# Kernel optimization log

Measured on AMD Instinct MI355X. Metric: run time of the kernel, lower is better.

Reference implementation:

```python
import jax, jax.numpy as jnp
import numpy as np

EPS = 1e-4
HEADS = 8
DIM_HEAD = 32
BALANCE = 0.3


def _normalize(x, dims):
    # torch normalize(): norm over `dims` in fp32; norm = eps + norm*sqrt(norm.numel()/x.numel())
    red = 1
    for d in dims:
        red *= x.shape[d]
    norm = jnp.sqrt(jnp.sum(jnp.square(x.astype(jnp.float32)), axis=dims, keepdims=True))
    norm = EPS + norm / np.sqrt(red)
    return x / norm.astype(x.dtype)


def _mpconv1x1(x, w, gain=1.0):
    # MPConv forward (eval mode): weight-normalize per output channel, scale, 1x1 conv
    w = w.astype(jnp.float32)
    w = _normalize(w, (1, 2, 3))
    fan_in = w.shape[1] * w.shape[2] * w.shape[3]
    w = (w * (gain / np.sqrt(fan_in))).astype(x.dtype)[:, :, 0, 0]  # [out, in]
    return jnp.einsum('oi,nihw->nohw', w, x)


def setup_inputs() -> dict:
    key = jax.random.key(0)
    k1, k2, k3 = jax.random.split(key, 3)
    x = jax.random.normal(k1, (2, 256, 48, 48), dtype=jnp.float32)
    w_qkv = jax.random.normal(k2, (768, 256, 1, 1), dtype=jnp.float32)
    w_out = jax.random.normal(k3, (256, 256, 1, 1), dtype=jnp.float32)
    return {"x": x, "w_qkv": w_qkv, "w_out": w_out}


def reference(x, w_qkv, w_out):
    n, c, h, w_sp = x.shape
    seq = h * w_sp
    y = _mpconv1x1(x, w_qkv)                          # [n, 3c, h, w]
    y = y.reshape(n, HEADS, DIM_HEAD, 3, seq)         # channel split: head x dim_head x 3
    y = _normalize(y, (2,))                           # L2-normalize over dim_head axis
    q = y[:, :, :, 0, :]
    k = y[:, :, :, 1, :]
    v = y[:, :, :, 2, :]
    # scores [n, h, q, k] with k scaled by 1/sqrt(dim_head)
    att = jax.nn.softmax(jnp.einsum('nhcq,nhck->nhqk', q, k) / np.sqrt(DIM_HEAD), axis=3)
    y = jnp.einsum('nhqk,nhck->nhcq', att, v)         # [n, heads, dim_head, seq]
    y = _mpconv1x1(y.reshape(n, c, h, w_sp), w_out)
    t = BALANCE
    # mp_sum: lerp then magnitude-preserving rescale
    return (x + t * (y - x)) / np.sqrt((1 - t) ** 2 + t ** 2)
```

## Files before the change

### kernel.cpp

```cpp
#include <hip/hip_runtime.h>
#include <math.h>

#define EPSN 1e-4f
#define SEQ 2304

using bf16x8 = __attribute__((ext_vector_type(8))) short;
using f32x4  = __attribute__((ext_vector_type(4))) float;

__device__ inline unsigned short f2bf(float x) {
    union { float f; unsigned u; } c; c.f = x;
    unsigned u = c.u;
    u += 0x7fffu + ((u >> 16) & 1u);
    return (unsigned short)(u >> 16);
}

__device__ inline unsigned cvt_pk_bf16(float lo, float hi) {
    unsigned r;
    asm("v_cvt_pk_bf16_f32 %0, %1, %2" : "=v"(r) : "v"(lo), "v"(hi));
    return r;
}
__device__ inline void permlane32_swap(unsigned &a, unsigned &b) {
    asm("v_permlane32_swap_b32 %0, %1" : "+v"(a), "+v"(b));
}
__device__ inline void permlane16_swap(unsigned &a, unsigned &b) {
    asm("v_permlane16_swap_b32 %0, %1" : "+v"(a), "+v"(b));
}

__global__ __launch_bounds__(256) void prep_kernel(const float* __restrict__ w_qkv,
                                                   const float* __restrict__ w_out,
                                                   const float* __restrict__ x,
                                                   unsigned short* __restrict__ wqb,
                                                   unsigned short* __restrict__ wob,
                                                   unsigned short* __restrict__ xt) {
    __shared__ __align__(16) unsigned short T[64][80];
    int bid = blockIdx.x;
    if (bid < 256) {
        int wave = threadIdx.x >> 6, lane = threadIdx.x & 63;
        int row = bid * 4 + wave;
        const float* src;
        unsigned short* dst;
        if (row < 768) { src = w_qkv + (size_t)row * 256; dst = wqb + (size_t)row * 256; }
        else           { src = w_out + (size_t)(row - 768) * 256; dst = wob + (size_t)(row - 768) * 256; }
        float4 v = *(const float4*)&src[lane * 4];
        float ss = v.x * v.x + v.y * v.y + v.z * v.z + v.w * v.w;
        for (int off = 32; off > 0; off >>= 1) ss += __shfl_xor(ss, off, 64);
        float sc = 1.0f / (sqrtf(ss) + 16.0f * EPSN);
        unsigned p0 = (unsigned)f2bf(v.x * sc) | ((unsigned)f2bf(v.y * sc) << 16);
        unsigned p1 = (unsigned)f2bf(v.z * sc) | ((unsigned)f2bf(v.w * sc) << 16);
        *(uint2*)&dst[lane * 4] = make_uint2(p0, p1);
    } else {
        int e0 = bid - 256;
        int st = e0 % 36, ct = (e0 / 36) & 3, n = e0 / 144;
        int t = threadIdx.x;
#pragma unroll
        for (int p = 0; p < 4; ++p) {
            int e = t + p * 256;
            int c = e >> 4, sv = (e & 15) * 4;
            float4 v = *(const float4*)&x[(size_t)(n * 256 + ct * 64 + c) * SEQ + st * 64 + sv];
            T[sv + 0][c] = f2bf(v.x);
            T[sv + 1][c] = f2bf(v.y);
            T[sv + 2][c] = f2bf(v.z);
            T[sv + 3][c] = f2bf(v.w);
        }
        __syncthreads();
#pragma unroll
        for (int p = 0; p < 2; ++p) {
            int e = t + p * 256;
            int s = e >> 3, cb = (e & 7) * 8;
            uint4 v = *(const uint4*)&T[s][cb];
            *(uint4*)&xt[(size_t)(n * SEQ + st * 64 + s) * 256 + ct * 64 + cb] = v;
        }
    }
}

__global__ __launch_bounds__(256) void qkv_fused_kernel(const unsigned short* __restrict__ xt,
                                                        const unsigned short* __restrict__ wqb,
                                                        unsigned short* __restrict__ qn,
                                                        unsigned short* __restrict__ kn,
                                                        unsigned short* __restrict__ vn) {
    __shared__ float Cs[96][65];
    __shared__ __align__(16) unsigned short Vls[32][72];
    int h  = blockIdx.x;
    int st = blockIdx.y;
    int n  = blockIdx.z;
    int tid = threadIdx.x;
    int wave = tid >> 6, lane = tid & 63;
    int ln = lane & 15, quad = lane >> 4;
    const unsigned short* Abase = wqb + (size_t)(h * 96 + ln) * 256 + quad * 8;
    const unsigned short* Bbase = xt + (size_t)(n * SEQ + st * 64 + wave * 16 + ln) * 256 + quad * 8;
    f32x4 acc[6];
#pragma unroll
    for (int m = 0; m < 6; ++m) acc[m] = (f32x4){0.f, 0.f, 0.f, 0.f};
#pragma unroll
    for (int kc = 0; kc < 8; ++kc) {
        bf16x8 b = *(const bf16x8*)(Bbase + kc * 32);
#pragma unroll
        for (int m = 0; m < 6; ++m) {
            bf16x8 a = *(const bf16x8*)(Abase + (size_t)(m * 16) * 256 + kc * 32);
            acc[m] = __builtin_amdgcn_mfma_f32_16x16x32_bf16(a, b, acc[m], 0, 0, 0);
        }
    }
#pragma unroll
    for (int m = 0; m < 6; ++m)
#pragma unroll
        for (int r = 0; r < 4; ++r)
            Cs[m * 16 + quad * 4 + r][wave * 16 + ln] = acc[m][r];
    __syncthreads();
    int nh = n * 8 + h;
    if (tid < 192) {
        int sl = tid & 63, wh = tid >> 6;
        int s = st * 64 + sl;
        float v[32];
        float ss = 0.f;
#pragma unroll
        for (int d = 0; d < 32; ++d) { v[d] = Cs[3 * d + wh][sl]; ss += v[d] * v[d]; }
        float inv = 1.0f / (EPSN + sqrtf(ss * (1.0f / 32.0f)));
        if (wh == 0) inv *= 0.17677669529663687f * 1.4426950408889634f;
        if (wh == 2) {
#pragma unroll
            for (int d = 0; d < 32; ++d) Vls[d][sl] = f2bf(v[d] * inv);
        } else {
            unsigned short* dst = (wh == 1 ? kn : qn) + (size_t)nh * 73728 + (size_t)s * 32;
            unsigned wbuf[16];
#pragma unroll
            for (int j = 0; j < 16; ++j)
                wbuf[j] = (unsigned)f2bf(v[2 * j] * inv) | ((unsigned)f2bf(v[2 * j + 1] * inv) << 16);
#pragma unroll
            for (int j = 0; j < 4; ++j) {
                uint4 t4 = make_uint4(wbuf[4 * j], wbuf[4 * j + 1], wbuf[4 * j + 2], wbuf[4 * j + 3]);
                *(uint4*)(dst + j * 8) = t4;
            }
        }
    }
    __syncthreads();
    {
        int d = tid >> 3, sj = (tid & 7) * 8;
        uint4 t4 = *(const uint4*)&Vls[d][sj];
        *(uint4*)&vn[(size_t)nh * 73728 + (size_t)d * SEQ + st * 64 + sj] = t4;
    }
}

__global__ __launch_bounds__(512) void attn_mfma_kernel(const unsigned short* __restrict__ qn,
                                                        const unsigned short* __restrict__ kn,
                                                        const unsigned short* __restrict__ vn,
                                                        unsigned short* __restrict__ y2t) {
    __shared__ __align__(16) unsigned char SM[38912];
    unsigned short (*Ks)[64][40] = (unsigned short (*)[64][40])SM;
    unsigned short (*Vs)[32][72] = (unsigned short (*)[32][72])(SM + 20480);
    int tid = threadIdx.x;
    int wave = tid >> 6, lane = tid & 63;
    int ln = lane & 15, quad = lane >> 4;
    int kg = wave >> 2, wq = wave & 3;
    int bid = blockIdx.x;
    int xcd = bid & 7, bi = bid >> 3;
    int nh = xcd * 2 + (bi >= 36);
    int qt = (bi >= 36) ? bi - 36 : bi;
    int n = nh >> 3, h = nh & 7;
    const unsigned short* Qg = qn + (size_t)nh * 73728;
    const unsigned short* Kg = kn + (size_t)nh * 73728;
    const unsigned short* Vg = vn + (size_t)nh * 73728;

    bf16x8 qf = *(const bf16x8*)(Qg + (size_t)(qt * 64 + wq * 16 + ln) * 32 + quad * 8);
    bf16x8 ones;
#pragma unroll
    for (int i = 0; i < 8; ++i) ones[i] = (short)0x3F80;

    f32x4 o0 = {0.f, 0.f, 0.f, 0.f};
    f32x4 o1 = {0.f, 0.f, 0.f, 0.f};
    f32x4 lac = {0.f, 0.f, 0.f, 0.f};

    int ts = tid & 255;
    int kg2 = kg * 2;
    int s0 = kg * 18 * 64;
    uint4 kreg = *(const uint4*)(Kg + (size_t)s0 * 32 + ts * 8);
    uint4 vreg = *(const uint4*)(Vg + (size_t)(ts >> 3) * SEQ + s0 + (ts & 7) * 8);
    *(uint4*)(&Ks[kg2][ts >> 2][(ts & 3) * 8]) = kreg;
    *(uint4*)(&Vs[kg2][ts >> 3][(ts & 7) * 8]) = vreg;

    for (int i = 0; i < 18; ++i) {
        int buf = i & 1;
        if (i + 1 < 18) {
            int sn = s0 + (i + 1) * 64;
            kreg = *(const uint4*)(Kg + (size_t)sn * 32 + ts * 8);
            vreg = *(const uint4*)(Vg + (size_t)(ts >> 3) * SEQ + sn + (ts & 7) * 8);
        }
        __syncthreads();

        const f32x4 zero = {0.f, 0.f, 0.f, 0.f};
        unsigned w[4][2];
#pragma unroll
        for (int c = 0; c < 4; ++c) {
            bf16x8 kf = *(const bf16x8*)(&Ks[kg2 + buf][c * 16 + ln][quad * 8]);
            f32x4 sc = __builtin_amdgcn_mfma_f32_16x16x32_bf16(kf, qf, zero, 0, 0, 0);
            w[c][0] = cvt_pk_bf16(exp2f(sc[0]), exp2f(sc[1]));
            w[c][1] = cvt_pk_bf16(exp2f(sc[2]), exp2f(sc[3]));
        }
#pragma unroll
        for (int kc = 0; kc < 2; ++kc) {
            unsigned a0 = w[2 * kc][0], b0 = w[2 * kc + 1][0];
            permlane32_swap(a0, b0);
            permlane16_swap(a0, b0);
            unsigned a1 = w[2 * kc][1], b1 = w[2 * kc + 1][1];
            permlane32_swap(a1, b1);
            permlane16_swap(a1, b1);
            union { unsigned u[4]; bf16x8 v8; } pk;
            pk.u[0] = a0; pk.u[1] = a1; pk.u[2] = b0; pk.u[3] = b1;
            bf16x8 v0 = *(const bf16x8*)(&Vs[kg2 + buf][ln][kc * 32 + quad * 8]);
            bf16x8 v1 = *(const bf16x8*)(&Vs[kg2 + buf][16 + ln][kc * 32 + quad * 8]);
            lac = __builtin_amdgcn_mfma_f32_16x16x32_bf16(pk.v8, ones, lac, 0, 0, 0);
            o0  = __builtin_amdgcn_mfma_f32_16x16x32_bf16(pk.v8, v0, o0, 0, 0, 0);
            o1  = __builtin_amdgcn_mfma_f32_16x16x32_bf16(pk.v8, v1, o1, 0, 0, 0);
        }
        if (i + 1 < 18) {
            *(uint4*)(&Ks[kg2 + (buf ^ 1)][ts >> 2][(ts & 3) * 8]) = kreg;
            *(uint4*)(&Vs[kg2 + (buf ^ 1)][ts >> 3][(ts & 7) * 8]) = vreg;
        }
    }

    __syncthreads();
    float (*Os)[36] = (float (*)[36])SM;
    float* Ls = (float*)(SM + 128 * 36 * 4);
#pragma unroll
    for (int r = 0; r < 4; ++r) {
        int q = wq * 16 + quad * 4 + r;
        Os[kg * 64 + q][ln] = o0[r];
        Os[kg * 64 + q][16 + ln] = o1[r];
        if (ln == 0) Ls[kg * 64 + q] = lac[r];
    }
    __syncthreads();
    {
        int q = tid >> 3, dg = (tid & 7) * 4;
        float inv = 1.0f / (Ls[q] + Ls[64 + q]);
        float r0 = (Os[q][dg + 0] + Os[64 + q][dg + 0]) * inv;
        float r1 = (Os[q][dg + 1] + Os[64 + q][dg + 1]) * inv;
        float r2 = (Os[q][dg + 2] + Os[64 + q][dg + 2]) * inv;
        float r3 = (Os[q][dg + 3] + Os[64 + q][dg + 3]) * inv;
        *(uint2*)&y2t[((size_t)(n * SEQ) + qt * 64 + q) * 256 + h * 32 + dg] =
            make_uint2(cvt_pk_bf16(r0, r1), cvt_pk_bf16(r2, r3));
    }
}

__global__ __launch_bounds__(256) void out_gemm_kernel(const unsigned short* __restrict__ y2t,
                                                       const unsigned short* __restrict__ wob,
                                                       const float* __restrict__ x,
                                                       float* __restrict__ out) {
    int mt = blockIdx.x;
    int st = blockIdx.y;
    int n  = blockIdx.z;
    int tid = threadIdx.x;
    int wave = tid >> 6, lane = tid & 63;
    int ln = lane & 15, quad = lane >> 4;
    int m0 = mt * 64 + wave * 16;
    const unsigned short* Abase = wob + (size_t)(m0 + ln) * 256 + quad * 8;
    const unsigned short* Bbase = y2t + (size_t)(n * SEQ + st * 32 + ln) * 256 + quad * 8;
    f32x4 acc[2];
#pragma unroll
    for (int c = 0; c < 2; ++c) acc[c] = (f32x4){0.f, 0.f, 0.f, 0.f};
#pragma unroll
    for (int kc = 0; kc < 8; ++kc) {
        bf16x8 a = *(const bf16x8*)(Abase + kc * 32);
#pragma unroll
        for (int c = 0; c < 2; ++c) {
            bf16x8 b = *(const bf16x8*)(Bbase + (size_t)(c * 16) * 256 + kc * 32);
            acc[c] = __builtin_amdgcn_mfma_f32_16x16x32_bf16(a, b, acc[c], 0, 0, 0);
        }
    }
    const float c0f = 0.7f * 1.3130643285972254f;
    const float c1f = 0.3f * 1.3130643285972254f;
#pragma unroll
    for (int c = 0; c < 2; ++c)
#pragma unroll
        for (int r = 0; r < 4; ++r) {
            int o = m0 + quad * 4 + r;
            int s = st * 32 + c * 16 + ln;
            size_t idx = (size_t)(n * 256 + o) * SEQ + s;
            out[idx] = c0f * x[idx] + c1f * acc[c][r];
        }
}

extern "C" void kernel_launch(void* const* d_in, const int* in_sizes, int n_in,
                              void* d_out, int out_size, void* d_ws, size_t ws_size,
                              hipStream_t stream) {
    (void)in_sizes; (void)n_in; (void)out_size; (void)ws_size;
    const float* x     = (const float*)d_in[0];
    const float* w_qkv = (const float*)d_in[1];
    const float* w_out = (const float*)d_in[2];
    float* out = (float*)d_out;
    float* ws  = (float*)d_ws;
    unsigned short* wqb = (unsigned short*)(ws);
    unsigned short* wob = (unsigned short*)(ws + 98304);
    unsigned short* xt  = (unsigned short*)(ws + 131072);
    unsigned short* y2t = (unsigned short*)(ws + 131072);
    unsigned short* qn  = (unsigned short*)(ws + 720896);
    unsigned short* kn  = (unsigned short*)(ws + 1310720);
    unsigned short* vn  = (unsigned short*)(ws + 1900544);

    hipLaunchKernelGGL(prep_kernel, dim3(544), dim3(256), 0, stream,
                       w_qkv, w_out, x, wqb, wob, xt);
    hipLaunchKernelGGL(qkv_fused_kernel, dim3(8, 36, 2), dim3(256), 0, stream,
                       xt, wqb, qn, kn, vn);
    hipLaunchKernelGGL(attn_mfma_kernel, dim3(576), dim3(512), 0, stream,
                       qn, kn, vn, y2t);
    hipLaunchKernelGGL(out_gemm_kernel, dim3(4, 72, 2), dim3(256), 0, stream,
                       y2t, wob, x, out);
}
```

Baseline: 133.7 us.

## Remap grids for XCD locality, unroll attention loop by two, sum softmax denominators in VALU

```diff
diff --git a/kernel.cpp b/kernel.cpp
--- a/kernel.cpp
+++ b/kernel.cpp
@@ -80,9 +80,11 @@
                                                         unsigned short* __restrict__ vn) {
     __shared__ float Cs[96][65];
     __shared__ __align__(16) unsigned short Vls[32][72];
-    int h  = blockIdx.x;
-    int st = blockIdx.y;
-    int n  = blockIdx.z;
+    int bid = blockIdx.x;
+    int xcd = bid & 7, j = bid >> 3;
+    int h = j & 7;
+    int tilej = xcd * 9 + (j >> 3);
+    int st = tilej % 36, n = tilej / 36;
     int tid = threadIdx.x;
     int wave = tid >> 6, lane = tid & 63;
     int ln = lane & 15, quad = lane >> 4;
@@ -123,12 +125,12 @@
             unsigned short* dst = (wh == 1 ? kn : qn) + (size_t)nh * 73728 + (size_t)s * 32;
             unsigned wbuf[16];
 #pragma unroll
-            for (int j = 0; j < 16; ++j)
-                wbuf[j] = (unsigned)f2bf(v[2 * j] * inv) | ((unsigned)f2bf(v[2 * j + 1] * inv) << 16);
-#pragma unroll
-            for (int j = 0; j < 4; ++j) {
-                uint4 t4 = make_uint4(wbuf[4 * j], wbuf[4 * j + 1], wbuf[4 * j + 2], wbuf[4 * j + 3]);
-                *(uint4*)(dst + j * 8) = t4;
+            for (int j2 = 0; j2 < 16; ++j2)
+                wbuf[j2] = (unsigned)f2bf(v[2 * j2] * inv) | ((unsigned)f2bf(v[2 * j2 + 1] * inv) << 16);
+#pragma unroll
+            for (int j2 = 0; j2 < 4; ++j2) {
+                uint4 t4 = make_uint4(wbuf[4 * j2], wbuf[4 * j2 + 1], wbuf[4 * j2 + 2], wbuf[4 * j2 + 3]);
+                *(uint4*)(dst + j2 * 8) = t4;
             }
         }
     }
@@ -161,39 +163,27 @@
     const unsigned short* Vg = vn + (size_t)nh * 73728;
 
     bf16x8 qf = *(const bf16x8*)(Qg + (size_t)(qt * 64 + wq * 16 + ln) * 32 + quad * 8);
-    bf16x8 ones;
-#pragma unroll
-    for (int i = 0; i < 8; ++i) ones[i] = (short)0x3F80;
 
     f32x4 o0 = {0.f, 0.f, 0.f, 0.f};
     f32x4 o1 = {0.f, 0.f, 0.f, 0.f};
-    f32x4 lac = {0.f, 0.f, 0.f, 0.f};
+    float lsum = 0.f;
 
     int ts = tid & 255;
     int kg2 = kg * 2;
     int s0 = kg * 18 * 64;
-    uint4 kreg = *(const uint4*)(Kg + (size_t)s0 * 32 + ts * 8);
-    uint4 vreg = *(const uint4*)(Vg + (size_t)(ts >> 3) * SEQ + s0 + (ts & 7) * 8);
-    *(uint4*)(&Ks[kg2][ts >> 2][(ts & 3) * 8]) = kreg;
-    *(uint4*)(&Vs[kg2][ts >> 3][(ts & 7) * 8]) = vreg;
-
-    for (int i = 0; i < 18; ++i) {
-        int buf = i & 1;
-        if (i + 1 < 18) {
-            int sn = s0 + (i + 1) * 64;
-            kreg = *(const uint4*)(Kg + (size_t)sn * 32 + ts * 8);
-            vreg = *(const uint4*)(Vg + (size_t)(ts >> 3) * SEQ + sn + (ts & 7) * 8);
-        }
-        __syncthreads();
-
+
+    auto compute_tile = [&](int bsel) {
         const f32x4 zero = {0.f, 0.f, 0.f, 0.f};
         unsigned w[4][2];
 #pragma unroll
         for (int c = 0; c < 4; ++c) {
-            bf16x8 kf = *(const bf16x8*)(&Ks[kg2 + buf][c * 16 + ln][quad * 8]);
+            bf16x8 kf = *(const bf16x8*)(&Ks[bsel][c * 16 + ln][quad * 8]);
             f32x4 sc = __builtin_amdgcn_mfma_f32_16x16x32_bf16(kf, qf, zero, 0, 0, 0);
-            w[c][0] = cvt_pk_bf16(exp2f(sc[0]), exp2f(sc[1]));
-            w[c][1] = cvt_pk_bf16(exp2f(sc[2]), exp2f(sc[3]));
+            float e0 = exp2f(sc[0]), e1 = exp2f(sc[1]);
+            float e2 = exp2f(sc[2]), e3 = exp2f(sc[3]);
+            lsum += (e0 + e1) + (e2 + e3);
+            w[c][0] = cvt_pk_bf16(e0, e1);
+            w[c][1] = cvt_pk_bf16(e2, e3);
         }
 #pragma unroll
         for (int kc = 0; kc < 2; ++kc) {
@@ -205,17 +195,45 @@
             permlane16_swap(a1, b1);
             union { unsigned u[4]; bf16x8 v8; } pk;
             pk.u[0] = a0; pk.u[1] = a1; pk.u[2] = b0; pk.u[3] = b1;
-            bf16x8 v0 = *(const bf16x8*)(&Vs[kg2 + buf][ln][kc * 32 + quad * 8]);
-            bf16x8 v1 = *(const bf16x8*)(&Vs[kg2 + buf][16 + ln][kc * 32 + quad * 8]);
-            lac = __builtin_amdgcn_mfma_f32_16x16x32_bf16(pk.v8, ones, lac, 0, 0, 0);
-            o0  = __builtin_amdgcn_mfma_f32_16x16x32_bf16(pk.v8, v0, o0, 0, 0, 0);
-            o1  = __builtin_amdgcn_mfma_f32_16x16x32_bf16(pk.v8, v1, o1, 0, 0, 0);
-        }
-        if (i + 1 < 18) {
-            *(uint4*)(&Ks[kg2 + (buf ^ 1)][ts >> 2][(ts & 3) * 8]) = kreg;
-            *(uint4*)(&Vs[kg2 + (buf ^ 1)][ts >> 3][(ts & 7) * 8]) = vreg;
-        }
-    }
+            bf16x8 v0 = *(const bf16x8*)(&Vs[bsel][ln][kc * 32 + quad * 8]);
+            bf16x8 v1 = *(const bf16x8*)(&Vs[bsel][16 + ln][kc * 32 + quad * 8]);
+            o0 = __builtin_amdgcn_mfma_f32_16x16x32_bf16(pk.v8, v0, o0, 0, 0, 0);
+            o1 = __builtin_amdgcn_mfma_f32_16x16x32_bf16(pk.v8, v1, o1, 0, 0, 0);
+        }
+    };
+
+    uint4 kA = *(const uint4*)(Kg + (size_t)s0 * 32 + ts * 8);
+    uint4 vA = *(const uint4*)(Vg + (size_t)(ts >> 3) * SEQ + s0 + (ts & 7) * 8);
+    *(uint4*)(&Ks[kg2][ts >> 2][(ts & 3) * 8]) = kA;
+    *(uint4*)(&Vs[kg2][ts >> 3][(ts & 7) * 8]) = vA;
+    uint4 kB = *(const uint4*)(Kg + (size_t)(s0 + 64) * 32 + ts * 8);
+    uint4 vB = *(const uint4*)(Vg + (size_t)(ts >> 3) * SEQ + (s0 + 64) + (ts & 7) * 8);
+
+    for (int i = 0; i < 18; i += 2) {
+        if (i + 2 < 18) {
+            int sn = s0 + (i + 2) * 64;
+            kA = *(const uint4*)(Kg + (size_t)sn * 32 + ts * 8);
+            vA = *(const uint4*)(Vg + (size_t)(ts >> 3) * SEQ + sn + (ts & 7) * 8);
+        }
+        __syncthreads();
+        compute_tile(kg2);
+        *(uint4*)(&Ks[kg2 + 1][ts >> 2][(ts & 3) * 8]) = kB;
+        *(uint4*)(&Vs[kg2 + 1][ts >> 3][(ts & 7) * 8]) = vB;
+        if (i + 3 < 18) {
+            int sn = s0 + (i + 3) * 64;
+            kB = *(const uint4*)(Kg + (size_t)sn * 32 + ts * 8);
+            vB = *(const uint4*)(Vg + (size_t)(ts >> 3) * SEQ + sn + (ts & 7) * 8);
+        }
+        __syncthreads();
+        compute_tile(kg2 + 1);
+        if (i + 2 < 18) {
+            *(uint4*)(&Ks[kg2][ts >> 2][(ts & 3) * 8]) = kA;
+            *(uint4*)(&Vs[kg2][ts >> 3][(ts & 7) * 8]) = vA;
+        }
+    }
+
+    lsum += __shfl_xor(lsum, 16, 64);
+    lsum += __shfl_xor(lsum, 32, 64);
 
     __syncthreads();
     float (*Os)[36] = (float (*)[36])SM;
@@ -225,8 +243,8 @@
         int q = wq * 16 + quad * 4 + r;
         Os[kg * 64 + q][ln] = o0[r];
         Os[kg * 64 + q][16 + ln] = o1[r];
-        if (ln == 0) Ls[kg * 64 + q] = lac[r];
-    }
+    }
+    if (quad == 0) Ls[kg * 64 + wq * 16 + ln] = lsum;
     __syncthreads();
     {
         int q = tid >> 3, dg = (tid & 7) * 4;
@@ -244,8 +262,8 @@
                                                        const unsigned short* __restrict__ wob,
                                                        const float* __restrict__ x,
                                                        float* __restrict__ out) {
-    int mt = blockIdx.x;
-    int st = blockIdx.y;
+    int st = blockIdx.x;
+    int mt = blockIdx.y;
     int n  = blockIdx.z;
     int tid = threadIdx.x;
     int wave = tid >> 6, lane = tid & 63;
@@ -297,10 +315,10 @@
 
     hipLaunchKernelGGL(prep_kernel, dim3(544), dim3(256), 0, stream,
                        w_qkv, w_out, x, wqb, wob, xt);
-    hipLaunchKernelGGL(qkv_fused_kernel, dim3(8, 36, 2), dim3(256), 0, stream,
+    hipLaunchKernelGGL(qkv_fused_kernel, dim3(576), dim3(256), 0, stream,
                        xt, wqb, qn, kn, vn);
     hipLaunchKernelGGL(attn_mfma_kernel, dim3(576), dim3(512), 0, stream,
                        qn, kn, vn, y2t);
-    hipLaunchKernelGGL(out_gemm_kernel, dim3(4, 72, 2), dim3(256), 0, stream,
+    hipLaunchKernelGGL(out_gemm_kernel, dim3(72, 4, 2), dim3(256), 0, stream,
                        y2t, wob, x, out);
 }
```

Result: no change. 134.8 us (+0.8%).
